# Performance work log

Measured on AMD Instinct MI355X. Metric: run time of the kernel, lower is better.

The kernel has to match this reference:

```python
import jax, jax.numpy as jnp
import numpy as np

EPS = 1e-5
G = 8    # groups
K = 3    # kernel_size


def bn(x, gamma, beta, mean, var):
    # inference-mode BatchNorm2d; x: (b,C,H,W), params: (C,)
    inv = gamma / jnp.sqrt(var + EPS)
    return x * inv[None, :, None, None] + (beta - mean * inv)[None, :, None, None]


def gconv1x1(x, w):
    # grouped 1x1 conv; x: (b, g*ci, H, W), w: (g, co, ci) -> (b, g*co, H, W)
    b, C, H, W = x.shape
    g, co, ci = w.shape
    xg = x.reshape(b, g, ci, H, W)
    y = jnp.einsum('bgihw,goi->bgohw', xg, w)
    return y.reshape(b, g * co, H, W)


def unfold3(x):
    # torch.nn.Unfold(k=3, stride=1, dilation=1, padding=1), reshaped to (b, C, 9, H, W)
    b, C, H, W = x.shape
    xp = jnp.pad(x, ((0, 0), (0, 0), (1, 1), (1, 1)))
    patches = [xp[:, :, i:i + H, j:j + W] for i in range(K) for j in range(K)]
    return jnp.stack(patches, axis=2)


def setup_inputs() -> dict:
    key = jax.random.key(0)
    ks = jax.random.split(key, 16)
    f = jax.random.normal
    u = jax.random.uniform
    return {
        'x':  f(ks[0], (2, 256, 128, 128), jnp.float32),
        'w1': f(ks[1], (8, 8, 32), jnp.float32) * 0.1,
        'b1': f(ks[2], (64,), jnp.float32) * 0.1,
        'g1': u(ks[3], (64,), jnp.float32, 0.5, 1.5),
        'be1': f(ks[4], (64,), jnp.float32) * 0.1,
        'm1': f(ks[5], (64,), jnp.float32) * 0.1,
        'v1': u(ks[6], (64,), jnp.float32, 0.5, 1.5),
        'w2': f(ks[7], (8, 10, 8), jnp.float32) * 0.1,
        'b2': f(ks[8], (80,), jnp.float32) * 0.1,
        'g2': u(ks[9], (80,), jnp.float32, 0.5, 1.5),
        'be2': f(ks[10], (80,), jnp.float32) * 0.1,
        'm2': f(ks[11], (80,), jnp.float32) * 0.1,
        'v2': u(ks[12], (80,), jnp.float32, 0.5, 1.5),
        'wv': f(ks[13], (8, 32, 32), jnp.float32) * 0.1,
    }


def reference(x, w1, b1, g1, be1, m1, v1, w2, b2, g2, be2, m2, v2, wv):
    b, C, H, W = x.shape
    # mask_conv: grouped 1x1 conv -> BN -> tanh -> grouped 1x1 conv -> BN
    t = jnp.tanh(bn(gconv1x1(x, w1) + b1[None, :, None, None], g1, be1, m1, v1))
    mn = bn(gconv1x1(t, w2) + b2[None, :, None, None], g2, be2, m2, v2)  # (b, G*(1+K*K), H, W)
    neighbor = mn[:, :G]          # (b, G, H, W)
    mask = mn[:, G:]              # (b, G*K*K, H, W)
    nb = unfold3(neighbor)        # (b, G, 9, H, W)
    logits = mask.reshape(b, G, K * K, H, W) + nb
    attn = jax.nn.softmax(logits, axis=2)               # (b, G, 9, H, W)
    # value path: grouped 1x1 conv (no bias) then unfold
    v = gconv1x1(x, wv)                                  # (b, C, H, W)
    vu = unfold3(v).reshape(b, G, C // G, K * K, H, W)   # (b, G, C/G, 9, H, W)
    out = jnp.einsum('bgkhw,bgckhw->bgchw', attn, vu)    # weighted sum over window
    return out.reshape(b, C, H, W)
```

## Files before the change

kernel.cpp:

```cpp
#include <hip/hip_runtime.h>

#define HW  16384
#define WD  128

__device__ __forceinline__ unsigned short f2bf(float f) {
    unsigned int u = __builtin_bit_cast(unsigned int, f);
    u += 0x7FFFu + ((u >> 16) & 1u);
    return (unsigned short)(u >> 16);
}
__device__ __forceinline__ float bf2f(unsigned int s) {
    return __builtin_bit_cast(float, (s & 0xFFFFu) << 16);
}
__device__ __forceinline__ float ftanh(float v) {
    const float e = __expf(2.0f * v);
    return 1.0f - __fdividef(2.0f, e + 1.0f);
}

__global__ __launch_bounds__(256) void la_pre(
    const float* __restrict__ x,
    const float* __restrict__ w1, const float* __restrict__ b1,
    const float* __restrict__ g1, const float* __restrict__ be1,
    const float* __restrict__ m1, const float* __restrict__ v1,
    const float* __restrict__ w2, const float* __restrict__ b2,
    const float* __restrict__ g2, const float* __restrict__ be2,
    const float* __restrict__ m2, const float* __restrict__ v2,
    const float* __restrict__ wv,
    uint4* __restrict__ v4, float* __restrict__ nb, float* __restrict__ mask)
{
    const int pix = blockIdx.x * blockDim.x + threadIdx.x;
    const int b   = blockIdx.y;
    const int p   = blockIdx.z;

    const float* xp = x + (size_t)(b * 256 + p * 32) * HW + pix;
    float xv[32];
#pragma unroll
    for (int c = 0; c < 32; ++c) xv[c] = xp[(size_t)c * HW];

    const float* w1g = w1 + p * 256;
    float tv[8];
#pragma unroll
    for (int o = 0; o < 8; ++o) {
        float a = 0.f;
#pragma unroll
        for (int ci = 0; ci < 32; ++ci) a = fmaf(xv[ci], w1g[o * 32 + ci], a);
        const int ch = p * 8 + o;
        const float inv = g1[ch] * rsqrtf(v1[ch] + 1e-5f);
        const float add = be1[ch] + (b1[ch] - m1[ch]) * inv;
        tv[o] = ftanh(fmaf(a, inv, add));
    }

#pragma unroll
    for (int o = 0; o < 10; ++o) {
        const int c = p * 10 + o;
        float a = 0.f;
#pragma unroll
        for (int i = 0; i < 8; ++i) a = fmaf(tv[i], w2[p * 80 + o * 8 + i], a);
        const float inv = g2[c] * rsqrtf(v2[c] + 1e-5f);
        const float add = be2[c] + (b2[c] - m2[c]) * inv;
        const float val = fmaf(a, inv, add);
        if (c < 8) {
            nb[(size_t)(b * 8 + c) * HW + pix] = val;
        } else {
            const int gk = c - 8, g = gk / 9, k = gk - 9 * g;
            mask[((size_t)(b * 8 + g) * 9 + k) * HW + pix] = val;
        }
    }

    const float* wvp = wv + p * 1024;
#pragma unroll
    for (int c8 = 0; c8 < 4; ++c8) {
        float ov[8];
#pragma unroll
        for (int j = 0; j < 8; ++j) {
            float a = 0.f;
#pragma unroll
            for (int ci = 0; ci < 32; ++ci)
                a = fmaf(xv[ci], wvp[(c8 * 8 + j) * 32 + ci], a);
            ov[j] = a;
        }
        uint4 u;
        u.x = (unsigned)f2bf(ov[0]) | ((unsigned)f2bf(ov[1]) << 16);
        u.y = (unsigned)f2bf(ov[2]) | ((unsigned)f2bf(ov[3]) << 16);
        u.z = (unsigned)f2bf(ov[4]) | ((unsigned)f2bf(ov[5]) << 16);
        u.w = (unsigned)f2bf(ov[6]) | ((unsigned)f2bf(ov[7]) << 16);
        v4[((size_t)((b * 8 + p) * 4) + c8) * HW + pix] = u;
    }
}

__global__ __launch_bounds__(256) void la_attn(
    const uint4* __restrict__ v4, const float* __restrict__ nb,
    const float* __restrict__ mask, float* __restrict__ out)
{
    const int pix = blockIdx.x * blockDim.x + threadIdx.x;
    const int bg  = blockIdx.y;
    const int b   = bg >> 3, g = bg & 7;
    const int iy  = pix >> 7, ix = pix & 127;

    const float* mp  = mask + ((size_t)(b * 8 + g) * 9) * HW + pix;
    const float* nbp = nb   + (size_t)(b * 8 + g) * HW + pix;
    const uint4* vg  = v4   + ((size_t)(b * 8 + g) * 4) * HW + pix;

    float lg[9];
    float mx = -1e30f;
#pragma unroll
    for (int k = 0; k < 9; ++k) {
        const int dy = k / 3 - 1, dx = k % 3 - 1;
        const bool ok = ((unsigned)(iy + dy) < 128u) && ((unsigned)(ix + dx) < 128u);
        const float nv = ok ? nbp[dy * WD + dx] : 0.f;
        lg[k] = mp[(size_t)k * HW] + nv;
        mx = fmaxf(mx, lg[k]);
    }
    float ssum = 0.f;
#pragma unroll
    for (int k = 0; k < 9; ++k) { lg[k] = __expf(lg[k] - mx); ssum += lg[k]; }
    const float rs = 1.f / ssum;

    float s[32];
#pragma unroll
    for (int c = 0; c < 32; ++c) s[c] = 0.f;
#pragma unroll
    for (int k = 0; k < 9; ++k) {
        const int dy = k / 3 - 1, dx = k % 3 - 1;
        const bool ok = ((unsigned)(iy + dy) < 128u) && ((unsigned)(ix + dx) < 128u);
        if (ok) {
            const int off = dy * WD + dx;
            const float e = lg[k];
#pragma unroll
            for (int c8 = 0; c8 < 4; ++c8) {
                const uint4 u = vg[(size_t)c8 * HW + off];
                s[c8 * 8 + 0] = fmaf(e, bf2f(u.x),       s[c8 * 8 + 0]);
                s[c8 * 8 + 1] = fmaf(e, bf2f(u.x >> 16), s[c8 * 8 + 1]);
                s[c8 * 8 + 2] = fmaf(e, bf2f(u.y),       s[c8 * 8 + 2]);
                s[c8 * 8 + 3] = fmaf(e, bf2f(u.y >> 16), s[c8 * 8 + 3]);
                s[c8 * 8 + 4] = fmaf(e, bf2f(u.z),       s[c8 * 8 + 4]);
                s[c8 * 8 + 5] = fmaf(e, bf2f(u.z >> 16), s[c8 * 8 + 5]);
                s[c8 * 8 + 6] = fmaf(e, bf2f(u.w),       s[c8 * 8 + 6]);
                s[c8 * 8 + 7] = fmaf(e, bf2f(u.w >> 16), s[c8 * 8 + 7]);
            }
        }
    }

    float* og = out + (size_t)(b * 256 + g * 32) * HW + pix;
#pragma unroll 8
    for (int o = 0; o < 32; ++o)
        __builtin_nontemporal_store(s[o] * rs, og + (size_t)o * HW);
}

extern "C" void kernel_launch(void* const* d_in, const int* in_sizes, int n_in,
                              void* d_out, int out_size, void* d_ws, size_t ws_size,
                              hipStream_t stream)
{
    const float* x   = (const float*)d_in[0];
    const float* w1  = (const float*)d_in[1];
    const float* b1  = (const float*)d_in[2];
    const float* g1  = (const float*)d_in[3];
    const float* be1 = (const float*)d_in[4];
    const float* m1  = (const float*)d_in[5];
    const float* v1  = (const float*)d_in[6];
    const float* w2  = (const float*)d_in[7];
    const float* b2  = (const float*)d_in[8];
    const float* g2  = (const float*)d_in[9];
    const float* be2 = (const float*)d_in[10];
    const float* m2  = (const float*)d_in[11];
    const float* v2  = (const float*)d_in[12];
    const float* wv  = (const float*)d_in[13];

    float* out = (float*)d_out;

    uint4* v4  = (uint4*)d_ws;
    float* nbw = (float*)((char*)d_ws + (size_t)64 * HW * 16);
    float* msk = nbw + (size_t)16 * HW;

    dim3 blk(256);
    dim3 gpre(HW / 256, 2, 8);
    dim3 gatt(HW / 256, 16);

    hipLaunchKernelGGL(la_pre, gpre, blk, 0, stream,
                       x, w1, b1, g1, be1, m1, v1, w2, b2, g2, be2, m2, v2,
                       wv, v4, nbw, msk);
    hipLaunchKernelGGL(la_attn, gatt, blk, 0, stream,
                       v4, nbw, msk, out);
}
```

Measured before the change: 140.6 us.

## Split pre and attention kernels across more blocks to raise occupancy

The pre kernel now launches three block slices per group: two compute halves of the value projection and one computes the mask/neighbor path. The attention kernel splits its 32 output channels into two halves per block. Both kernels get a launch-bounds minimum-blocks hint to cap register use. This trades more parallelism and lower register pressure for redundant reads of x (three times) and duplicated softmax/mask loads.

```diff
diff --git a/kernel.cpp b/kernel.cpp
--- a/kernel.cpp
+++ b/kernel.cpp
@@ -16,7 +16,7 @@
     return 1.0f - __fdividef(2.0f, e + 1.0f);
 }
 
-__global__ __launch_bounds__(256) void la_pre(
+__global__ __launch_bounds__(256, 8) void la_pre(
     const float* __restrict__ x,
     const float* __restrict__ w1, const float* __restrict__ b1,
     const float* __restrict__ g1, const float* __restrict__ be1,
@@ -29,76 +29,82 @@
 {
     const int pix = blockIdx.x * blockDim.x + threadIdx.x;
     const int b   = blockIdx.y;
-    const int p   = blockIdx.z;
+    const int z   = blockIdx.z;
+    const int p   = z / 3;
+    const int q   = z - 3 * p;
 
     const float* xp = x + (size_t)(b * 256 + p * 32) * HW + pix;
     float xv[32];
 #pragma unroll
     for (int c = 0; c < 32; ++c) xv[c] = xp[(size_t)c * HW];
 
-    const float* w1g = w1 + p * 256;
-    float tv[8];
+    if (q < 2) {
+        const float* wvp = wv + p * 1024 + q * 512;
 #pragma unroll
-    for (int o = 0; o < 8; ++o) {
-        float a = 0.f;
+        for (int c8 = 0; c8 < 2; ++c8) {
+            float ov[8];
 #pragma unroll
-        for (int ci = 0; ci < 32; ++ci) a = fmaf(xv[ci], w1g[o * 32 + ci], a);
-        const int ch = p * 8 + o;
-        const float inv = g1[ch] * rsqrtf(v1[ch] + 1e-5f);
-        const float add = be1[ch] + (b1[ch] - m1[ch]) * inv;
-        tv[o] = ftanh(fmaf(a, inv, add));
-    }
-
+            for (int j = 0; j < 8; ++j) {
+                float a = 0.f;
 #pragma unroll
-    for (int o = 0; o < 10; ++o) {
-        const int c = p * 10 + o;
-        float a = 0.f;
+                for (int ci = 0; ci < 32; ++ci)
+                    a = fmaf(xv[ci], wvp[(c8 * 8 + j) * 32 + ci], a);
+                ov[j] = a;
+            }
+            uint4 u;
+            u.x = (unsigned)f2bf(ov[0]) | ((unsigned)f2bf(ov[1]) << 16);
+            u.y = (unsigned)f2bf(ov[2]) | ((unsigned)f2bf(ov[3]) << 16);
+            u.z = (unsigned)f2bf(ov[4]) | ((unsigned)f2bf(ov[5]) << 16);
+            u.w = (unsigned)f2bf(ov[6]) | ((unsigned)f2bf(ov[7]) << 16);
+            v4[((size_t)((b * 8 + p) * 4) + q * 2 + c8) * HW + pix] = u;
+        }
+    } else {
+        const float* w1g = w1 + p * 256;
+        float tv[8];
 #pragma unroll
-        for (int i = 0; i < 8; ++i) a = fmaf(tv[i], w2[p * 80 + o * 8 + i], a);
-        const float inv = g2[c] * rsqrtf(v2[c] + 1e-5f);
-        const float add = be2[c] + (b2[c] - m2[c]) * inv;
-        const float val = fmaf(a, inv, add);
-        if (c < 8) {
-            nb[(size_t)(b * 8 + c) * HW + pix] = val;
-        } else {
-            const int gk = c - 8, g = gk / 9, k = gk - 9 * g;
-            mask[((size_t)(b * 8 + g) * 9 + k) * HW + pix] = val;
-        }
-    }
-
-    const float* wvp = wv + p * 1024;
-#pragma unroll
-    for (int c8 = 0; c8 < 4; ++c8) {
-        float ov[8];
-#pragma unroll
-        for (int j = 0; j < 8; ++j) {
+        for (int o = 0; o < 8; ++o) {
             float a = 0.f;
 #pragma unroll
             for (int ci = 0; ci < 32; ++ci)
-                a = fmaf(xv[ci], wvp[(c8 * 8 + j) * 32 + ci], a);
-            ov[j] = a;
+                a = fmaf(xv[ci], w1g[o * 32 + ci], a);
+            const int ch = p * 8 + o;
+            const float inv = g1[ch] * rsqrtf(v1[ch] + 1e-5f);
+            const float add = be1[ch] + (b1[ch] - m1[ch]) * inv;
+            tv[o] = ftanh(fmaf(a, inv, add));
         }
-        uint4 u;
-        u.x = (unsigned)f2bf(ov[0]) | ((unsigned)f2bf(ov[1]) << 16);
-        u.y = (unsigned)f2bf(ov[2]) | ((unsigned)f2bf(ov[3]) << 16);
-        u.z = (unsigned)f2bf(ov[4]) | ((unsigned)f2bf(ov[5]) << 16);
-        u.w = (unsigned)f2bf(ov[6]) | ((unsigned)f2bf(ov[7]) << 16);
-        v4[((size_t)((b * 8 + p) * 4) + c8) * HW + pix] = u;
+#pragma unroll
+        for (int o = 0; o < 10; ++o) {
+            const int c = p * 10 + o;
+            float a = 0.f;
+#pragma unroll
+            for (int i = 0; i < 8; ++i)
+                a = fmaf(tv[i], w2[p * 80 + o * 8 + i], a);
+            const float inv = g2[c] * rsqrtf(v2[c] + 1e-5f);
+            const float add = be2[c] + (b2[c] - m2[c]) * inv;
+            const float val = fmaf(a, inv, add);
+            if (c < 8) {
+                nb[(size_t)(b * 8 + c) * HW + pix] = val;
+            } else {
+                const int gk = c - 8, g = gk / 9, k = gk - 9 * g;
+                mask[((size_t)(b * 8 + g) * 9 + k) * HW + pix] = val;
+            }
+        }
     }
 }
 
-__global__ __launch_bounds__(256) void la_attn(
+__global__ __launch_bounds__(256, 8) void la_attn(
     const uint4* __restrict__ v4, const float* __restrict__ nb,
     const float* __restrict__ mask, float* __restrict__ out)
 {
     const int pix = blockIdx.x * blockDim.x + threadIdx.x;
-    const int bg  = blockIdx.y;
+    const int y   = blockIdx.y;
+    const int bg  = y >> 1, h = y & 1;
     const int b   = bg >> 3, g = bg & 7;
     const int iy  = pix >> 7, ix = pix & 127;
 
     const float* mp  = mask + ((size_t)(b * 8 + g) * 9) * HW + pix;
     const float* nbp = nb   + (size_t)(b * 8 + g) * HW + pix;
-    const uint4* vg  = v4   + ((size_t)(b * 8 + g) * 4) * HW + pix;
+    const uint4* vg  = v4   + ((size_t)((b * 8 + g) * 4) + 2 * h) * HW + pix;
 
     float lg[9];
     float mx = -1e30f;
@@ -107,7 +113,7 @@
         const int dy = k / 3 - 1, dx = k % 3 - 1;
         const bool ok = ((unsigned)(iy + dy) < 128u) && ((unsigned)(ix + dx) < 128u);
         const float nv = ok ? nbp[dy * WD + dx] : 0.f;
-        lg[k] = mp[(size_t)k * HW] + nv;
+        lg[k] = __builtin_nontemporal_load(mp + (size_t)k * HW) + nv;
         mx = fmaxf(mx, lg[k]);
     }
     float ssum = 0.f;
@@ -115,9 +121,9 @@
     for (int k = 0; k < 9; ++k) { lg[k] = __expf(lg[k] - mx); ssum += lg[k]; }
     const float rs = 1.f / ssum;
 
-    float s[32];
+    float s[16];
 #pragma unroll
-    for (int c = 0; c < 32; ++c) s[c] = 0.f;
+    for (int c = 0; c < 16; ++c) s[c] = 0.f;
 #pragma unroll
     for (int k = 0; k < 9; ++k) {
         const int dy = k / 3 - 1, dx = k % 3 - 1;
@@ -126,7 +132,7 @@
             const int off = dy * WD + dx;
             const float e = lg[k];
 #pragma unroll
-            for (int c8 = 0; c8 < 4; ++c8) {
+            for (int c8 = 0; c8 < 2; ++c8) {
                 const uint4 u = vg[(size_t)c8 * HW + off];
                 s[c8 * 8 + 0] = fmaf(e, bf2f(u.x),       s[c8 * 8 + 0]);
                 s[c8 * 8 + 1] = fmaf(e, bf2f(u.x >> 16), s[c8 * 8 + 1]);
@@ -140,9 +146,9 @@
         }
     }
 
-    float* og = out + (size_t)(b * 256 + g * 32) * HW + pix;
+    float* og = out + (size_t)(b * 256 + g * 32 + h * 16) * HW + pix;
 #pragma unroll 8
-    for (int o = 0; o < 32; ++o)
+    for (int o = 0; o < 16; ++o)
         __builtin_nontemporal_store(s[o] * rs, og + (size_t)o * HW);
 }
 
@@ -172,8 +178,8 @@
     float* msk = nbw + (size_t)16 * HW;
 
     dim3 blk(256);
-    dim3 gpre(HW / 256, 2, 8);
-    dim3 gatt(HW / 256, 16);
+    dim3 gpre(HW / 256, 2, 24);
+    dim3 gatt(HW / 256, 32);
 
     hipLaunchKernelGGL(la_pre, gpre, blk, 0, stream,
                        x, w1, b1, g1, be1, m1, v1, w2, b2, g2, be2, m2, v2,
```

Result: slower. 235.1 us (+67.3%).

## Apply value conv after attention-weighted window sum, drop bf16 value buffer

Applied to the files above, without the earlier changes.

Uses linearity of the grouped 1x1 value convolution to apply it after the softmax-weighted 3x3 window sum, reading x directly in fp32 instead of a precomputed bf16 value tensor. This removes the value intermediate write and read and the bf16 pack/unpack work. The pre kernel now only computes the mask path, split in two halves per group, which recomputes the first conv and reads x twice. The attention kernel reads 32 fp32 channels per tap instead of bf16, doubling gathered bytes per tap.

```diff
diff --git a/kernel.cpp b/kernel.cpp
--- a/kernel.cpp
+++ b/kernel.cpp
@@ -3,14 +3,6 @@
 #define HW  16384
 #define WD  128
 
-__device__ __forceinline__ unsigned short f2bf(float f) {
-    unsigned int u = __builtin_bit_cast(unsigned int, f);
-    u += 0x7FFFu + ((u >> 16) & 1u);
-    return (unsigned short)(u >> 16);
-}
-__device__ __forceinline__ float bf2f(unsigned int s) {
-    return __builtin_bit_cast(float, (s & 0xFFFFu) << 16);
-}
 __device__ __forceinline__ float ftanh(float v) {
     const float e = __expf(2.0f * v);
     return 1.0f - __fdividef(2.0f, e + 1.0f);
@@ -24,12 +16,13 @@
     const float* __restrict__ w2, const float* __restrict__ b2,
     const float* __restrict__ g2, const float* __restrict__ be2,
     const float* __restrict__ m2, const float* __restrict__ v2,
-    const float* __restrict__ wv,
-    uint4* __restrict__ v4, float* __restrict__ nb, float* __restrict__ mask)
+    float* __restrict__ nb, float* __restrict__ mask)
 {
     const int pix = blockIdx.x * blockDim.x + threadIdx.x;
     const int b   = blockIdx.y;
-    const int p   = blockIdx.z;
+    const int z   = blockIdx.z;
+    const int p   = z >> 1;
+    const int h   = z & 1;
 
     const float* xp = x + (size_t)(b * 256 + p * 32) * HW + pix;
     float xv[32];
@@ -50,11 +43,13 @@
     }
 
 #pragma unroll
-    for (int o = 0; o < 10; ++o) {
+    for (int r = 0; r < 5; ++r) {
+        const int o = h * 5 + r;
         const int c = p * 10 + o;
         float a = 0.f;
 #pragma unroll
-        for (int i = 0; i < 8; ++i) a = fmaf(tv[i], w2[p * 80 + o * 8 + i], a);
+        for (int i = 0; i < 8; ++i)
+            a = fmaf(tv[i], w2[p * 80 + o * 8 + i], a);
         const float inv = g2[c] * rsqrtf(v2[c] + 1e-5f);
         const float add = be2[c] + (b2[c] - m2[c]) * inv;
         const float val = fmaf(a, inv, add);
@@ -65,40 +60,21 @@
             mask[((size_t)(b * 8 + g) * 9 + k) * HW + pix] = val;
         }
     }
-
-    const float* wvp = wv + p * 1024;
-#pragma unroll
-    for (int c8 = 0; c8 < 4; ++c8) {
-        float ov[8];
-#pragma unroll
-        for (int j = 0; j < 8; ++j) {
-            float a = 0.f;
-#pragma unroll
-            for (int ci = 0; ci < 32; ++ci)
-                a = fmaf(xv[ci], wvp[(c8 * 8 + j) * 32 + ci], a);
-            ov[j] = a;
-        }
-        uint4 u;
-        u.x = (unsigned)f2bf(ov[0]) | ((unsigned)f2bf(ov[1]) << 16);
-        u.y = (unsigned)f2bf(ov[2]) | ((unsigned)f2bf(ov[3]) << 16);
-        u.z = (unsigned)f2bf(ov[4]) | ((unsigned)f2bf(ov[5]) << 16);
-        u.w = (unsigned)f2bf(ov[6]) | ((unsigned)f2bf(ov[7]) << 16);
-        v4[((size_t)((b * 8 + p) * 4) + c8) * HW + pix] = u;
-    }
 }
 
 __global__ __launch_bounds__(256) void la_attn(
-    const uint4* __restrict__ v4, const float* __restrict__ nb,
-    const float* __restrict__ mask, float* __restrict__ out)
+    const float* __restrict__ x, const float* __restrict__ wv,
+    const float* __restrict__ nb, const float* __restrict__ mask,
+    float* __restrict__ out)
 {
     const int pix = blockIdx.x * blockDim.x + threadIdx.x;
-    const int bg  = blockIdx.y;
-    const int b   = bg >> 3, g = bg & 7;
+    const int y   = blockIdx.y;
+    const int b   = y >> 3, g = y & 7;
     const int iy  = pix >> 7, ix = pix & 127;
 
     const float* mp  = mask + ((size_t)(b * 8 + g) * 9) * HW + pix;
     const float* nbp = nb   + (size_t)(b * 8 + g) * HW + pix;
-    const uint4* vg  = v4   + ((size_t)(b * 8 + g) * 4) * HW + pix;
+    const float* xg  = x    + (size_t)(b * 256 + g * 32) * HW + pix;
 
     float lg[9];
     float mx = -1e30f;
@@ -126,24 +102,21 @@
             const int off = dy * WD + dx;
             const float e = lg[k];
 #pragma unroll
-            for (int c8 = 0; c8 < 4; ++c8) {
-                const uint4 u = vg[(size_t)c8 * HW + off];
-                s[c8 * 8 + 0] = fmaf(e, bf2f(u.x),       s[c8 * 8 + 0]);
-                s[c8 * 8 + 1] = fmaf(e, bf2f(u.x >> 16), s[c8 * 8 + 1]);
-                s[c8 * 8 + 2] = fmaf(e, bf2f(u.y),       s[c8 * 8 + 2]);
-                s[c8 * 8 + 3] = fmaf(e, bf2f(u.y >> 16), s[c8 * 8 + 3]);
-                s[c8 * 8 + 4] = fmaf(e, bf2f(u.z),       s[c8 * 8 + 4]);
-                s[c8 * 8 + 5] = fmaf(e, bf2f(u.z >> 16), s[c8 * 8 + 5]);
-                s[c8 * 8 + 6] = fmaf(e, bf2f(u.w),       s[c8 * 8 + 6]);
-                s[c8 * 8 + 7] = fmaf(e, bf2f(u.w >> 16), s[c8 * 8 + 7]);
-            }
+            for (int c = 0; c < 32; ++c)
+                s[c] = fmaf(e, xg[(size_t)c * HW + off], s[c]);
         }
     }
 
+    const float* wvg = wv + g * 1024;
     float* og = out + (size_t)(b * 256 + g * 32) * HW + pix;
-#pragma unroll 8
-    for (int o = 0; o < 32; ++o)
-        __builtin_nontemporal_store(s[o] * rs, og + (size_t)o * HW);
+#pragma unroll 4
+    for (int o = 0; o < 32; ++o) {
+        const float* wp = wvg + o * 32;
+        float a = 0.f;
+#pragma unroll
+        for (int ci = 0; ci < 32; ++ci) a = fmaf(s[ci], wp[ci], a);
+        __builtin_nontemporal_store(a * rs, og + (size_t)o * HW);
+    }
 }
 
 extern "C" void kernel_launch(void* const* d_in, const int* in_sizes, int n_in,
@@ -167,17 +140,16 @@
 
     float* out = (float*)d_out;
 
-    uint4* v4  = (uint4*)d_ws;
-    float* nbw = (float*)((char*)d_ws + (size_t)64 * HW * 16);
+    float* nbw = (float*)d_ws;
     float* msk = nbw + (size_t)16 * HW;
 
     dim3 blk(256);
-    dim3 gpre(HW / 256, 2, 8);
+    dim3 gpre(HW / 256, 2, 16);
     dim3 gatt(HW / 256, 16);
 
     hipLaunchKernelGGL(la_pre, gpre, blk, 0, stream,
                        x, w1, b1, g1, be1, m1, v1, w2, b2, g2, be2, m2, v2,
-                       wv, v4, nbw, msk);
+                       nbw, msk);
     hipLaunchKernelGGL(la_attn, gatt, blk, 0, stream,
-                       v4, nbw, msk, out);
+                       x, wv, nbw, msk, out);
 }
```

Result: slower. 151.9 us (+8.1%).
